# Optimization experiments

Hardware: AMD Instinct MI355X
Metric: run time of the kernel (lower is better)

## Reference

```python
import jax, jax.numpy as jnp
import numpy as np

B, Q, C, H, L, P, DFF, EXTRA = 4, 64, 384, 6, 5, 4, 1024, 128
SIZES = [(14, 14), (28, 28), (56, 56), (112, 112), (224, 224)]
S = sum(h * w for h, w in SIZES)
DH = C // H


def setup_inputs() -> dict:
    key = jax.random.key(0)
    ks = iter(jax.random.split(key, 64))
    rn = lambda shape, s=1.0: jax.random.normal(next(ks), shape, jnp.float32) * s
    inp = dict(
        tgt=rn((B, Q, C)),
        reference_points=jax.random.uniform(next(ks), (B, Q, 2), dtype=jnp.float32),
        src=rn((B, S, C)),
        extra_memory=rn((B, EXTRA, C)),
        src_valid_ratios=jnp.ones((B, L, 2), jnp.float32),
        src_spatial_shapes=jnp.asarray(SIZES, jnp.int32),
        src_level_start_index=jnp.asarray(np.cumsum([0] + [h * w for h, w in SIZES])[:-1], jnp.int32),
    )
    for name, shape in [("sa_in_w", (3 * C, C)), ("sa_out_w", (C, C)),
                        ("ea_in_w", (3 * C, C)), ("ea_out_w", (C, C)),
                        ("ms_off_w", (H * L * P * 2, C)), ("ms_attn_w", (H * L * P, C)),
                        ("ms_val_w", (C, C)), ("ms_out_w", (C, C)),
                        ("ffn_w1", (DFF, C)), ("ffn_w2", (C, DFF))]:
        inp[name] = rn(shape, 0.02)
    for name, n in [("sa_in_b", 3 * C), ("sa_out_b", C), ("ea_in_b", 3 * C), ("ea_out_b", C),
                    ("ms_attn_b", H * L * P), ("ms_val_b", C), ("ms_out_b", C),
                    ("ffn_b1", DFF), ("ffn_b2", C),
                    ("ln2_b", C), ("lne_b", C), ("ln1_b", C), ("ln3_b", C)]:
        inp[name] = jnp.zeros((n,), jnp.float32)
    inp["ms_off_b"] = rn((H * L * P * 2,), 0.5)  # nonzero so sampling is off-grid
    for name in ["ln2_g", "lne_g", "ln1_g", "ln3_g"]:
        inp[name] = jnp.ones((C,), jnp.float32)
    return inp


def layer_norm(x, g, b, eps=1e-5):
    mu = x.mean(-1, keepdims=True)
    var = ((x - mu) ** 2).mean(-1, keepdims=True)
    return (x - mu) / jnp.sqrt(var + eps) * g + b


def mha(q_in, k_in, v_in, in_w, in_b, out_w, out_b):
    d = q_in.shape[-1]
    wq, wk, wv = in_w[:d], in_w[d:2 * d], in_w[2 * d:]
    bq, bk, bv = in_b[:d], in_b[d:2 * d], in_b[2 * d:]
    proj = lambda x, w, bias: (x @ w.T + bias).reshape(x.shape[0], x.shape[1], H, DH)
    q = proj(q_in, wq, bq)
    k = proj(k_in, wk, bk)
    v = proj(v_in, wv, bv)
    scores = jnp.einsum('bqhd,bkhd->bhqk', q, k) * (1.0 / np.sqrt(DH))
    a = jax.nn.softmax(scores, axis=-1)
    o = jnp.einsum('bhqk,bkhd->bqhd', a, v).reshape(q_in.shape[0], q_in.shape[1], d)
    return o @ out_w.T + out_b


def bilinear_sample(img, x, y):
    # img [N,Hh,Ww,D]; x,y [N,M] in pixel coords; zeros padding (grid_sample align_corners=False)
    N, Hh, Ww, D = img.shape
    x0 = jnp.floor(x)
    y0 = jnp.floor(y)
    wx = (x - x0)[..., None]
    wy = (y - y0)[..., None]
    rows = jnp.arange(N)[:, None]

    def g(xi, yi):
        valid = (xi >= 0) & (xi <= Ww - 1) & (yi >= 0) & (yi <= Hh - 1)
        xc = jnp.clip(xi, 0, Ww - 1).astype(jnp.int32)
        yc = jnp.clip(yi, 0, Hh - 1).astype(jnp.int32)
        return img[rows, yc, xc] * valid[..., None]

    v00 = g(x0, y0)
    v01 = g(x0 + 1, y0)
    v10 = g(x0, y0 + 1)
    v11 = g(x0 + 1, y0 + 1)
    top = v00 * (1 - wx) + v01 * wx
    bot = v10 * (1 - wx) + v11 * wx
    return top * (1 - wy) + bot * wy


def ms_deform_attn(query, ref_pts, src, spatial, lsi,
                   off_w, off_b, aw_w, aw_b, val_w, val_b, out_w, out_b):
    # query [B,Q,C], ref_pts [B,Q,L,2] normalized
    value = (src @ val_w.T + val_b).reshape(B, S, H, DH)
    off = (query @ off_w.T + off_b).reshape(B, Q, H, L, P, 2)
    aw = jax.nn.softmax((query @ aw_w.T + aw_b).reshape(B, Q, H, L * P), -1).reshape(B, Q, H, L, P)
    normalizer = jnp.asarray([[w_, h_] for h_, w_ in spatial], jnp.float32)  # [L,2] (W,H)
    loc = ref_pts[:, :, None, :, None, :] + off / normalizer[None, None, None, :, None, :]
    out = jnp.zeros((B, Q, H, DH), jnp.float32)
    for l, (h_, w_) in enumerate(spatial):
        h_, w_ = int(h_), int(w_)
        s0 = int(lsi[l])
        v_l = value[:, s0:s0 + h_ * w_].transpose(0, 2, 1, 3).reshape(B * H, h_, w_, DH)
        xy = loc[:, :, :, l].transpose(0, 2, 1, 3, 4).reshape(B * H, Q * P, 2)
        x = xy[..., 0] * w_ - 0.5
        y = xy[..., 1] * h_ - 0.5
        samp = bilinear_sample(v_l, x, y).reshape(B, H, Q, P, DH)
        out = out + jnp.einsum('bhqpd,bqhp->bqhd', samp, aw[:, :, :, l])
    return out.reshape(B, Q, C) @ out_w.T + out_b


def reference(tgt, reference_points, src, extra_memory, src_valid_ratios,
              src_spatial_shapes, src_level_start_index,
              sa_in_w, sa_in_b, sa_out_w, sa_out_b,
              ea_in_w, ea_in_b, ea_out_w, ea_out_b,
              ms_off_w, ms_off_b, ms_attn_w, ms_attn_b,
              ms_val_w, ms_val_b, ms_out_w, ms_out_b,
              ffn_w1, ffn_b1, ffn_w2, ffn_b2,
              ln2_g, ln2_b, lne_g, lne_b, ln1_g, ln1_b, ln3_g, ln3_b):
    spatial = np.asarray(jax.device_get(src_spatial_shapes))
    lsi = np.asarray(jax.device_get(src_level_start_index))
    # reference_points_input = ref[:, :, None] * valid_ratios[:, None] -> [B,Q,L,2]
    rp_in = reference_points[:, :, None] * src_valid_ratios[:, None]
    # self attention (query_pos is None)
    t2 = mha(tgt, tgt, tgt, sa_in_w, sa_in_b, sa_out_w, sa_out_b)
    tgt = layer_norm(tgt + t2, ln2_g, ln2_b)
    # extra cross attention over concatenated first/previous memory
    t2 = mha(tgt, extra_memory, extra_memory, ea_in_w, ea_in_b, ea_out_w, ea_out_b)
    tgt = layer_norm(tgt + t2, lne_g, lne_b)
    # multi-scale deformable cross attention
    t2 = ms_deform_attn(tgt, rp_in, src, spatial, lsi,
                        ms_off_w, ms_off_b, ms_attn_w, ms_attn_b,
                        ms_val_w, ms_val_b, ms_out_w, ms_out_b)
    tgt = layer_norm(tgt + t2, ln1_g, ln1_b)
    # FFN
    t2 = jax.nn.relu(tgt @ ffn_w1.T + ffn_b1) @ ffn_w2.T + ffn_b2
    tgt = layer_norm(tgt + t2, ln3_g, ln3_b)
    return tgt
```

## Files before the change

### kernel.cpp

```cpp
#include <hip/hip_runtime.h>
#include <hip/hip_bf16.h>

#define B_ 4
#define Q_ 64
#define C_ 384
#define H_ 6
#define L_ 5
#define P_ 4
#define DFF_ 1024
#define EXTRA_ 128
#define DH_ 64
#define S_ 66836

#define FLAG_RELU 1
#define FLAG_RES 2

__device__ __forceinline__ float wave_sum(float v) {
    for (int off = 32; off; off >>= 1) v += __shfl_xor(v, off);
    return v;
}
__device__ __forceinline__ float wave_max(float v) {
    for (int off = 32; off; off >>= 1) v = fmaxf(v, __shfl_xor(v, off));
    return v;
}

__global__ __launch_bounds__(256) void lin16_kernel(
        const float* __restrict__ in, const float* __restrict__ W,
        const float* __restrict__ bias, const float* __restrict__ res,
        float* __restrict__ out, int K, int OUT, int flags) {
    extern __shared__ float xs[];
    int t = threadIdx.x;
    int r0 = blockIdx.y * 16;
    int K4 = K >> 2;
    const float4* in4 = reinterpret_cast<const float4*>(in + (size_t)r0 * K);
    float4* xs4 = reinterpret_cast<float4*>(xs);
    for (int i = t; i < 16 * K4; i += 256) xs4[i] = in4[i];
    __syncthreads();
    int j = blockIdx.x * 64 + (t & 63);
    int rg = t >> 6;
    if (j >= OUT) return;
    const float4* wp = reinterpret_cast<const float4*>(W + (size_t)j * K);
    const float4* x0 = reinterpret_cast<const float4*>(xs + (rg * 4 + 0) * K);
    const float4* x1 = reinterpret_cast<const float4*>(xs + (rg * 4 + 1) * K);
    const float4* x2 = reinterpret_cast<const float4*>(xs + (rg * 4 + 2) * K);
    const float4* x3 = reinterpret_cast<const float4*>(xs + (rg * 4 + 3) * K);
    float a0 = 0.f, a1 = 0.f, a2 = 0.f, a3 = 0.f;
#pragma unroll 4
    for (int k = 0; k < K4; ++k) {
        float4 w = wp[k];
        float4 v0 = x0[k], v1 = x1[k], v2 = x2[k], v3 = x3[k];
        a0 += w.x * v0.x + w.y * v0.y + w.z * v0.z + w.w * v0.w;
        a1 += w.x * v1.x + w.y * v1.y + w.z * v1.z + w.w * v1.w;
        a2 += w.x * v2.x + w.y * v2.y + w.z * v2.z + w.w * v2.w;
        a3 += w.x * v3.x + w.y * v3.y + w.z * v3.z + w.w * v3.w;
    }
    float bb = bias[j];
    float v[4] = {a0 + bb, a1 + bb, a2 + bb, a3 + bb};
    int orow = r0 + rg * 4;
#pragma unroll
    for (int i = 0; i < 4; ++i) {
        float o = v[i];
        if (flags & FLAG_RES) o += res[(size_t)(orow + i) * OUT + j];
        if (flags & FLAG_RELU) o = fmaxf(o, 0.f);
        out[(size_t)(orow + i) * OUT + j] = o;
    }
}

__global__ __launch_bounds__(256) void prep_kernel(
        const float* __restrict__ in, const float* __restrict__ Woff,
        const float* __restrict__ boff, const float* __restrict__ Wa,
        const float* __restrict__ ba, float* __restrict__ offs,
        float* __restrict__ lg) {
    extern __shared__ float xs[];
    int t = threadIdx.x;
    int r0 = blockIdx.y * 16;
    const float4* in4 = reinterpret_cast<const float4*>(in + (size_t)r0 * 384);
    float4* xs4 = reinterpret_cast<float4*>(xs);
    for (int i = t; i < 16 * 96; i += 256) xs4[i] = in4[i];
    __syncthreads();
    int j = blockIdx.x * 64 + (t & 63);
    int rg = t >> 6;
    if (j >= 360) return;
    const float4* wp;
    float bb;
    if (j < 240) { wp = reinterpret_cast<const float4*>(Woff + (size_t)j * 384); bb = boff[j]; }
    else         { wp = reinterpret_cast<const float4*>(Wa + (size_t)(j - 240) * 384); bb = ba[j - 240]; }
    const float4* x0 = reinterpret_cast<const float4*>(xs + (rg * 4 + 0) * 384);
    const float4* x1 = reinterpret_cast<const float4*>(xs + (rg * 4 + 1) * 384);
    const float4* x2 = reinterpret_cast<const float4*>(xs + (rg * 4 + 2) * 384);
    const float4* x3 = reinterpret_cast<const float4*>(xs + (rg * 4 + 3) * 384);
    float a0 = 0.f, a1 = 0.f, a2 = 0.f, a3 = 0.f;
#pragma unroll 4
    for (int k = 0; k < 96; ++k) {
        float4 w = wp[k];
        float4 v0 = x0[k], v1 = x1[k], v2 = x2[k], v3 = x3[k];
        a0 += w.x * v0.x + w.y * v0.y + w.z * v0.z + w.w * v0.w;
        a1 += w.x * v1.x + w.y * v1.y + w.z * v1.z + w.w * v1.w;
        a2 += w.x * v2.x + w.y * v2.y + w.z * v2.z + w.w * v2.w;
        a3 += w.x * v3.x + w.y * v3.y + w.z * v3.z + w.w * v3.w;
    }
    float v[4] = {a0 + bb, a1 + bb, a2 + bb, a3 + bb};
    int orow = r0 + rg * 4;
#pragma unroll
    for (int i = 0; i < 4; ++i) {
        if (j < 240) offs[(size_t)(orow + i) * 240 + j] = v[i];
        else         lg[(size_t)(orow + i) * 120 + (j - 240)] = v[i];
    }
}

__global__ __launch_bounds__(384) void sa_attn_kernel(const float* __restrict__ qkv,
                                                      float* __restrict__ o) {
    int row = blockIdx.x;
    int b = row >> 6;
    int t = threadIdx.x;
    int h = t >> 6, lane = t & 63;
    __shared__ float q_lds[384], a_lds[384];
    q_lds[t] = qkv[(size_t)row * 1152 + t];
    __syncthreads();
    const float* krow = qkv + (size_t)(b * 64 + lane) * 1152 + 384 + h * 64;
    float s = 0.f;
#pragma unroll 8
    for (int d = 0; d < 64; ++d) s += q_lds[h * 64 + d] * krow[d];
    s *= 0.125f;
    float m = wave_max(s);
    float e = __expf(s - m);
    float sum = wave_sum(e);
    a_lds[t] = e / sum;
    __syncthreads();
    float acc = 0.f;
#pragma unroll 4
    for (int k = 0; k < 64; ++k)
        acc += a_lds[h * 64 + k] * qkv[(size_t)(b * 64 + k) * 1152 + 768 + h * 64 + lane];
    o[(size_t)row * 384 + t] = acc;
}

__global__ __launch_bounds__(384) void ea_attn_kernel(const float* __restrict__ q,
                                                      const float* __restrict__ kv,
                                                      float* __restrict__ o) {
    int row = blockIdx.x;
    int b = row >> 6;
    int t = threadIdx.x;
    int h = t >> 6, lane = t & 63;
    __shared__ float q_lds[384], a_lds[768];
    q_lds[t] = q[(size_t)row * 384 + t];
    __syncthreads();
    const float* k0 = kv + (size_t)(b * 128 + lane) * 768 + h * 64;
    const float* k1 = k0 + (size_t)64 * 768;
    float s0 = 0.f, s1 = 0.f;
#pragma unroll 8
    for (int d = 0; d < 64; ++d) { float qd = q_lds[h * 64 + d]; s0 += qd * k0[d]; s1 += qd * k1[d]; }
    s0 *= 0.125f; s1 *= 0.125f;
    float m = wave_max(fmaxf(s0, s1));
    float e0 = __expf(s0 - m), e1 = __expf(s1 - m);
    float sum = wave_sum(e0 + e1);
    a_lds[h * 128 + lane] = e0 / sum;
    a_lds[h * 128 + 64 + lane] = e1 / sum;
    __syncthreads();
    float acc = 0.f;
#pragma unroll 4
    for (int k = 0; k < 128; ++k)
        acc += a_lds[h * 128 + k] * kv[(size_t)(b * 128 + k) * 768 + 384 + h * 64 + lane];
    o[(size_t)row * 384 + t] = acc;
}

__global__ __launch_bounds__(64) void ln_kernel(const float* __restrict__ z,
                                                const float* __restrict__ g,
                                                const float* __restrict__ beta,
                                                float* __restrict__ out) {
    int row = blockIdx.x;
    int t = threadIdx.x;
    float v[6];
    float mean = 0.f;
#pragma unroll
    for (int i = 0; i < 6; ++i) {
        v[i] = z[(size_t)row * C_ + t + i * 64];
        mean += v[i];
    }
    mean = wave_sum(mean) * (1.f / C_);
    float var = 0.f;
#pragma unroll
    for (int i = 0; i < 6; ++i) { float d = v[i] - mean; var += d * d; }
    var = wave_sum(var) * (1.f / C_);
    float inv = rsqrtf(var + 1e-5f);
#pragma unroll
    for (int i = 0; i < 6; ++i) {
        int c = t + i * 64;
        out[(size_t)row * C_ + c] = (v[i] - mean) * inv * g[c] + beta[c];
    }
}

__global__ __launch_bounds__(128) void ms_gather_kernel(
        const float* __restrict__ src, const float* __restrict__ refp,
        const float* __restrict__ vr, const float* __restrict__ offs,
        const float* __restrict__ lg, float* __restrict__ pagg,
        float* __restrict__ pwsum) {
    int l = blockIdx.x, h = blockIdx.y, row = blockIdx.z;
    int b = row >> 6;
    int t = threadIdx.x;
    const int lsi[5] = {0, 196, 980, 4116, 16660};
    const int whl[5] = {14, 28, 56, 112, 224};
    int wh = whl[l];
    float Wf = (float)wh;
    const float* lp = lg + (size_t)row * 120 + h * 20;
    float m = -1e30f;
#pragma unroll
    for (int k = 0; k < 20; ++k) m = fmaxf(m, lp[k]);
    float denom = 0.f;
#pragma unroll
    for (int k = 0; k < 20; ++k) denom += __expf(lp[k] - m);
    float dinv = 1.f / denom;
    float rpx = refp[row * 2 + 0] * vr[(b * 5 + l) * 2 + 0];
    float rpy = refp[row * 2 + 1] * vr[(b * 5 + l) * 2 + 1];
    const float* srcb = src + ((size_t)b * S_ + lsi[l]) * 384;
    float acc0 = 0.f, acc1 = 0.f, acc2 = 0.f, wsm = 0.f;
#pragma unroll
    for (int p = 0; p < 4; ++p) {
        int oidx = row * 240 + ((h * 5 + l) * 4 + p) * 2;
        float ox = offs[oidx], oy = offs[oidx + 1];
        float x = (rpx + ox / Wf) * Wf - 0.5f;
        float y = (rpy + oy / Wf) * Wf - 0.5f;
        float x0 = floorf(x), y0 = floorf(y);
        float wx = x - x0, wy = y - y0;
        float a = __expf(lp[l * 4 + p] - m) * dinv;
        float cw[4] = {(1.f - wx) * (1.f - wy), wx * (1.f - wy), (1.f - wx) * wy, wx * wy};
        float cx[4] = {x0, x0 + 1.f, x0, x0 + 1.f};
        float cy[4] = {y0, y0, y0 + 1.f, y0 + 1.f};
#pragma unroll
        for (int c2 = 0; c2 < 4; ++c2) {
            bool valid = (cx[c2] >= 0.f) && (cx[c2] <= Wf - 1.f) &&
                         (cy[c2] >= 0.f) && (cy[c2] <= Wf - 1.f);
            if (!valid) continue;
            float w = a * cw[c2];
            wsm += w;
            int xi = (int)cx[c2], yi = (int)cy[c2];
            const float* sp = srcb + (size_t)(yi * wh + xi) * 384;
            acc0 += w * sp[t];
            acc1 += w * sp[t + 128];
            acc2 += w * sp[t + 256];
        }
    }
    float* ap = pagg + ((size_t)(row * 6 + h) * 5 + l) * 384;
    ap[t] = acc0; ap[t + 128] = acc1; ap[t + 256] = acc2;
    if (t == 0) pwsum[(row * 6 + h) * 5 + l] = wsm;
}

__global__ __launch_bounds__(256) void valproj_kernel(
        const float* __restrict__ pagg, const float* __restrict__ pwsum,
        const float* __restrict__ Wv, const float* __restrict__ bv,
        float* __restrict__ val) {
    __shared__ float xs[16 * 384];
    __shared__ float ws16[16];
    int t = threadIdx.x;
    int h = blockIdx.x;
    int r0 = blockIdx.y * 16;
    float4* xs4 = reinterpret_cast<float4*>(xs);
    for (int i = t; i < 16 * 96; i += 256) {
        int row = i / 96, c4 = i % 96;
        const float4* pp = reinterpret_cast<const float4*>(pagg) +
                           ((size_t)((r0 + row) * 6 + h) * 5) * 96 + c4;
        float4 s = pp[0];
        float4 p1 = pp[96], p2 = pp[192], p3 = pp[288], p4 = pp[384];
        s.x += p1.x + p2.x + p3.x + p4.x;
        s.y += p1.y + p2.y + p3.y + p4.y;
        s.z += p1.z + p2.z + p3.z + p4.z;
        s.w += p1.w + p2.w + p3.w + p4.w;
        xs4[i] = s;
    }
    if (t < 16) {
        const float* pw = pwsum + ((size_t)(r0 + t) * 6 + h) * 5;
        ws16[t] = pw[0] + pw[1] + pw[2] + pw[3] + pw[4];
    }
    __syncthreads();
    int j = h * 64 + (t & 63);
    int rg = t >> 6;
    const float4* wp = reinterpret_cast<const float4*>(Wv + (size_t)j * 384);
    const float4* x0 = reinterpret_cast<const float4*>(xs + (rg * 4 + 0) * 384);
    const float4* x1 = reinterpret_cast<const float4*>(xs + (rg * 4 + 1) * 384);
    const float4* x2 = reinterpret_cast<const float4*>(xs + (rg * 4 + 2) * 384);
    const float4* x3 = reinterpret_cast<const float4*>(xs + (rg * 4 + 3) * 384);
    float a0 = 0.f, a1 = 0.f, a2 = 0.f, a3 = 0.f;
#pragma unroll 4
    for (int k = 0; k < 96; ++k) {
        float4 w = wp[k];
        float4 v0 = x0[k], v1 = x1[k], v2 = x2[k], v3 = x3[k];
        a0 += w.x * v0.x + w.y * v0.y + w.z * v0.z + w.w * v0.w;
        a1 += w.x * v1.x + w.y * v1.y + w.z * v1.z + w.w * v1.w;
        a2 += w.x * v2.x + w.y * v2.y + w.z * v2.z + w.w * v2.w;
        a3 += w.x * v3.x + w.y * v3.y + w.z * v3.z + w.w * v3.w;
    }
    float bb = bv[j];
    int orow = r0 + rg * 4;
    float acc[4] = {a0, a1, a2, a3};
#pragma unroll
    for (int i = 0; i < 4; ++i)
        val[(size_t)(orow + i) * 384 + j] = acc[i] + bb * ws16[rg * 4 + i];
}

extern "C" void kernel_launch(void* const* d_in, const int* in_sizes, int n_in,
                              void* d_out, int out_size, void* d_ws, size_t ws_size,
                              hipStream_t stream) {
    const float* tgt   = (const float*)d_in[0];
    const float* refp  = (const float*)d_in[1];
    const float* src   = (const float*)d_in[2];
    const float* extra = (const float*)d_in[3];
    const float* vr    = (const float*)d_in[4];
    const float* sa_in_w  = (const float*)d_in[7];
    const float* sa_out_w = (const float*)d_in[8];
    const float* ea_in_w  = (const float*)d_in[9];
    const float* ea_out_w = (const float*)d_in[10];
    const float* ms_off_w = (const float*)d_in[11];
    const float* ms_attn_w= (const float*)d_in[12];
    const float* ms_val_w = (const float*)d_in[13];
    const float* ms_out_w = (const float*)d_in[14];
    const float* ffn_w1   = (const float*)d_in[15];
    const float* ffn_w2   = (const float*)d_in[16];
    const float* sa_in_b  = (const float*)d_in[17];
    const float* sa_out_b = (const float*)d_in[18];
    const float* ea_in_b  = (const float*)d_in[19];
    const float* ea_out_b = (const float*)d_in[20];
    const float* ms_attn_b= (const float*)d_in[21];
    const float* ms_val_b = (const float*)d_in[22];
    const float* ms_out_b = (const float*)d_in[23];
    const float* ffn_b1   = (const float*)d_in[24];
    const float* ffn_b2   = (const float*)d_in[25];
    const float* ln2_b    = (const float*)d_in[26];
    const float* lne_b    = (const float*)d_in[27];
    const float* ln1_b    = (const float*)d_in[28];
    const float* ln3_b    = (const float*)d_in[29];
    const float* ms_off_b = (const float*)d_in[30];
    const float* ln2_g    = (const float*)d_in[31];
    const float* lne_g    = (const float*)d_in[32];
    const float* ln1_g    = (const float*)d_in[33];
    const float* ln3_g    = (const float*)d_in[34];

    float* ws = (float*)d_ws;
    float* s_qkv  = ws;
    float* s_eakv = ws + 294912;
    float* s_osa  = ws + 688128;
    float* s_z    = ws + 786432;
    float* s_t1   = ws + 884736;
    float* s_eaq  = ws + 983040;
    float* s_oea  = ws + 1081344;
    float* s_t2   = ws + 1179648;
    float* s_off  = ws + 1277952;
    float* s_lg   = ws + 1339392;
    float* s_pagg = ws + 1370112;
    float* s_pws  = ws + 4319232;
    float* s_val  = ws + 4326912;
    float* s_t3   = ws + 4425216;
    float* s_h1   = ws + 4523520;

    const size_t LDS384 = 16 * 384 * 4;
    const size_t LDS1024 = 16 * 1024 * 4;

    lin16_kernel<<<dim3(18, 16), 256, LDS384, stream>>>(tgt, sa_in_w, sa_in_b, nullptr, s_qkv, 384, 1152, 0);
    lin16_kernel<<<dim3(12, 32), 256, LDS384, stream>>>(extra, ea_in_w + (size_t)C_ * C_, ea_in_b + C_, nullptr, s_eakv, 384, 768, 0);
    sa_attn_kernel<<<dim3(256), dim3(384), 0, stream>>>(s_qkv, s_osa);
    lin16_kernel<<<dim3(6, 16), 256, LDS384, stream>>>(s_osa, sa_out_w, sa_out_b, tgt, s_z, 384, 384, FLAG_RES);
    ln_kernel<<<dim3(256), dim3(64), 0, stream>>>(s_z, ln2_g, ln2_b, s_t1);
    lin16_kernel<<<dim3(6, 16), 256, LDS384, stream>>>(s_t1, ea_in_w, ea_in_b, nullptr, s_eaq, 384, 384, 0);
    ea_attn_kernel<<<dim3(256), dim3(384), 0, stream>>>(s_eaq, s_eakv, s_oea);
    lin16_kernel<<<dim3(6, 16), 256, LDS384, stream>>>(s_oea, ea_out_w, ea_out_b, s_t1, s_z, 384, 384, FLAG_RES);
    ln_kernel<<<dim3(256), dim3(64), 0, stream>>>(s_z, lne_g, lne_b, s_t2);
    prep_kernel<<<dim3(6, 16), 256, LDS384, stream>>>(s_t2, ms_off_w, ms_off_b, ms_attn_w, ms_attn_b, s_off, s_lg);
    ms_gather_kernel<<<dim3(5, 6, 256), dim3(128), 0, stream>>>(src, refp, vr, s_off, s_lg, s_pagg, s_pws);
    valproj_kernel<<<dim3(6, 16), 256, 0, stream>>>(s_pagg, s_pws, ms_val_w, ms_val_b, s_val);
    lin16_kernel<<<dim3(6, 16), 256, LDS384, stream>>>(s_val, ms_out_w, ms_out_b, s_t2, s_z, 384, 384, FLAG_RES);
    ln_kernel<<<dim3(256), dim3(64), 0, stream>>>(s_z, ln1_g, ln1_b, s_t3);
    lin16_kernel<<<dim3(16, 16), 256, LDS384, stream>>>(s_t3, ffn_w1, ffn_b1, nullptr, s_h1, 384, 1024, FLAG_RELU);
    lin16_kernel<<<dim3(6, 16), 256, LDS1024, stream>>>(s_h1, ffn_w2, ffn_b2, s_t3, s_z, 1024, 384, FLAG_RES);
    ln_kernel<<<dim3(256), dim3(64), 0, stream>>>(s_z, ln3_g, ln3_b, (float*)d_out);
}
```

Before: 296.5 us.

## Fuse attention blocks with output projection, residual and layernorm into per-row kernels

Merges the self-attention and extra-memory input projections into one launch, and fuses each attention stage (query projection, attention, output projection, residual add, layernorm) into a single per-row kernel. It also merges the value projection, output projection and layernorm of the deformable attention into one per-row kernel. The goal is fewer launches and fewer round trips of intermediates through global memory. In exchange, each row block rereads the full 384x384 weight matrices, 256 blocks in total, with no reuse across rows, so weight traffic rises and the GEMV-style matmuls become less efficient.

Result: faster. 268.2 us (-9.5%).

```diff
diff --git a/kernel.cpp b/kernel.cpp
--- a/kernel.cpp
+++ b/kernel.cpp
@@ -23,30 +23,42 @@
     for (int off = 32; off; off >>= 1) v = fmaxf(v, __shfl_xor(v, off));
     return v;
 }
-
-__global__ __launch_bounds__(256) void lin16_kernel(
-        const float* __restrict__ in, const float* __restrict__ W,
-        const float* __restrict__ bias, const float* __restrict__ res,
-        float* __restrict__ out, int K, int OUT, int flags) {
-    extern __shared__ float xs[];
-    int t = threadIdx.x;
-    int r0 = blockIdx.y * 16;
-    int K4 = K >> 2;
-    const float4* in4 = reinterpret_cast<const float4*>(in + (size_t)r0 * K);
+__device__ __forceinline__ float block_sum6(float v, float* red, int t) {
+    v = wave_sum(v);
+    if ((t & 63) == 0) red[t >> 6] = v;
+    __syncthreads();
+    float s = red[0] + red[1] + red[2] + red[3] + red[4] + red[5];
+    __syncthreads();
+    return s;
+}
+
+__global__ __launch_bounds__(256) void proj_kernel(
+        const float* __restrict__ tgt, const float* __restrict__ extra,
+        const float* __restrict__ Wqkv, const float* __restrict__ bqkv,
+        const float* __restrict__ Wkv, const float* __restrict__ bkv,
+        float* __restrict__ qkv, float* __restrict__ eakv) {
+    __shared__ float xs[16 * 384];
+    int t = threadIdx.x;
+    int bx = blockIdx.x;
+    const float *in, *W, *bias;
+    float* out;
+    int OUT, r0, xt;
+    if (bx < 288) { xt = bx % 18; r0 = (bx / 18) * 16; in = tgt;   W = Wqkv; bias = bqkv; out = qkv;  OUT = 1152; }
+    else { int b2 = bx - 288; xt = b2 % 12; r0 = (b2 / 12) * 16; in = extra; W = Wkv;  bias = bkv;  out = eakv; OUT = 768; }
+    const float4* in4 = reinterpret_cast<const float4*>(in + (size_t)r0 * 384);
     float4* xs4 = reinterpret_cast<float4*>(xs);
-    for (int i = t; i < 16 * K4; i += 256) xs4[i] = in4[i];
-    __syncthreads();
-    int j = blockIdx.x * 64 + (t & 63);
+    for (int i = t; i < 16 * 96; i += 256) xs4[i] = in4[i];
+    __syncthreads();
+    int j = xt * 64 + (t & 63);
     int rg = t >> 6;
-    if (j >= OUT) return;
-    const float4* wp = reinterpret_cast<const float4*>(W + (size_t)j * K);
-    const float4* x0 = reinterpret_cast<const float4*>(xs + (rg * 4 + 0) * K);
-    const float4* x1 = reinterpret_cast<const float4*>(xs + (rg * 4 + 1) * K);
-    const float4* x2 = reinterpret_cast<const float4*>(xs + (rg * 4 + 2) * K);
-    const float4* x3 = reinterpret_cast<const float4*>(xs + (rg * 4 + 3) * K);
+    const float4* wp = reinterpret_cast<const float4*>(W + (size_t)j * 384);
+    const float4* x0 = reinterpret_cast<const float4*>(xs + (rg * 4 + 0) * 384);
+    const float4* x1 = reinterpret_cast<const float4*>(xs + (rg * 4 + 1) * 384);
+    const float4* x2 = reinterpret_cast<const float4*>(xs + (rg * 4 + 2) * 384);
+    const float4* x3 = reinterpret_cast<const float4*>(xs + (rg * 4 + 3) * 384);
     float a0 = 0.f, a1 = 0.f, a2 = 0.f, a3 = 0.f;
 #pragma unroll 4
-    for (int k = 0; k < K4; ++k) {
+    for (int k = 0; k < 96; ++k) {
         float4 w = wp[k];
         float4 v0 = x0[k], v1 = x1[k], v2 = x2[k], v3 = x3[k];
         a0 += w.x * v0.x + w.y * v0.y + w.z * v0.z + w.w * v0.w;
@@ -58,12 +70,101 @@
     float v[4] = {a0 + bb, a1 + bb, a2 + bb, a3 + bb};
     int orow = r0 + rg * 4;
 #pragma unroll
-    for (int i = 0; i < 4; ++i) {
-        float o = v[i];
-        if (flags & FLAG_RES) o += res[(size_t)(orow + i) * OUT + j];
-        if (flags & FLAG_RELU) o = fmaxf(o, 0.f);
-        out[(size_t)(orow + i) * OUT + j] = o;
-    }
+    for (int i = 0; i < 4; ++i) out[(size_t)(orow + i) * OUT + j] = v[i];
+}
+
+__global__ __launch_bounds__(384) void sa_fused_kernel(
+        const float* __restrict__ qkv, const float* __restrict__ res,
+        const float* __restrict__ Wo, const float* __restrict__ bo,
+        const float* __restrict__ g, const float* __restrict__ beta,
+        float* __restrict__ out) {
+    int row = blockIdx.x;
+    int b = row >> 6;
+    int t = threadIdx.x;
+    int h = t >> 6, lane = t & 63;
+    __shared__ float q_lds[384], a_lds[384], o_lds[384], red[8];
+    q_lds[t] = qkv[(size_t)row * 1152 + t];
+    __syncthreads();
+    const float* krow = qkv + (size_t)(b * 64 + lane) * 1152 + 384 + h * 64;
+    float s = 0.f;
+#pragma unroll 8
+    for (int d = 0; d < 64; ++d) s += q_lds[h * 64 + d] * krow[d];
+    s *= 0.125f;
+    float m = wave_max(s);
+    float e = __expf(s - m);
+    float sum = wave_sum(e);
+    a_lds[t] = e / sum;
+    __syncthreads();
+    float acc = 0.f;
+#pragma unroll 4
+    for (int k = 0; k < 64; ++k)
+        acc += a_lds[h * 64 + k] * qkv[(size_t)(b * 64 + k) * 1152 + 768 + h * 64 + lane];
+    o_lds[t] = acc;
+    __syncthreads();
+    const float* wp = Wo + (size_t)t * 384;
+    float v = bo[t] + res[(size_t)row * 384 + t];
+#pragma unroll 4
+    for (int k = 0; k < 384; k += 4) {
+        float4 w = *reinterpret_cast<const float4*>(wp + k);
+        v += w.x * o_lds[k] + w.y * o_lds[k + 1] + w.z * o_lds[k + 2] + w.w * o_lds[k + 3];
+    }
+    float mean = block_sum6(v, red, t) * (1.f / 384.f);
+    float d = v - mean;
+    float var = block_sum6(d * d, red, t) * (1.f / 384.f);
+    out[(size_t)row * 384 + t] = d * rsqrtf(var + 1e-5f) * g[t] + beta[t];
+}
+
+__global__ __launch_bounds__(384) void ea_fused_kernel(
+        const float* __restrict__ t1, const float* __restrict__ kv,
+        const float* __restrict__ Wq, const float* __restrict__ bq,
+        const float* __restrict__ Wo, const float* __restrict__ bo,
+        const float* __restrict__ g, const float* __restrict__ beta,
+        float* __restrict__ out) {
+    int row = blockIdx.x;
+    int b = row >> 6;
+    int t = threadIdx.x;
+    int h = t >> 6, lane = t & 63;
+    __shared__ float in_lds[384], q_lds[384], a_lds[768], o_lds[384], red[8];
+    in_lds[t] = t1[(size_t)row * 384 + t];
+    __syncthreads();
+    const float* wq = Wq + (size_t)t * 384;
+    float qv = bq[t];
+#pragma unroll 4
+    for (int k = 0; k < 384; k += 4) {
+        float4 w = *reinterpret_cast<const float4*>(wq + k);
+        qv += w.x * in_lds[k] + w.y * in_lds[k + 1] + w.z * in_lds[k + 2] + w.w * in_lds[k + 3];
+    }
+    q_lds[t] = qv;
+    __syncthreads();
+    const float* k0 = kv + (size_t)(b * 128 + lane) * 768 + h * 64;
+    const float* k1 = k0 + (size_t)64 * 768;
+    float s0 = 0.f, s1 = 0.f;
+#pragma unroll 8
+    for (int d = 0; d < 64; ++d) { float qd = q_lds[h * 64 + d]; s0 += qd * k0[d]; s1 += qd * k1[d]; }
+    s0 *= 0.125f; s1 *= 0.125f;
+    float m = wave_max(fmaxf(s0, s1));
+    float e0 = __expf(s0 - m), e1 = __expf(s1 - m);
+    float sum = wave_sum(e0 + e1);
+    a_lds[h * 128 + lane] = e0 / sum;
+    a_lds[h * 128 + 64 + lane] = e1 / sum;
+    __syncthreads();
+    float acc = 0.f;
+#pragma unroll 4
+    for (int k = 0; k < 128; ++k)
+        acc += a_lds[h * 128 + k] * kv[(size_t)(b * 128 + k) * 768 + 384 + h * 64 + lane];
+    o_lds[t] = acc;
+    __syncthreads();
+    const float* wo = Wo + (size_t)t * 384;
+    float v = bo[t] + in_lds[t];
+#pragma unroll 4
+    for (int k = 0; k < 384; k += 4) {
+        float4 w = *reinterpret_cast<const float4*>(wo + k);
+        v += w.x * o_lds[k] + w.y * o_lds[k + 1] + w.z * o_lds[k + 2] + w.w * o_lds[k + 3];
+    }
+    float mean = block_sum6(v, red, t) * (1.f / 384.f);
+    float d = v - mean;
+    float var = block_sum6(d * d, red, t) * (1.f / 384.f);
+    out[(size_t)row * 384 + t] = d * rsqrtf(var + 1e-5f) * g[t] + beta[t];
 }
 
 __global__ __launch_bounds__(256) void prep_kernel(
@@ -71,7 +172,7 @@
         const float* __restrict__ boff, const float* __restrict__ Wa,
         const float* __restrict__ ba, float* __restrict__ offs,
         float* __restrict__ lg) {
-    extern __shared__ float xs[];
+    __shared__ float xs[16 * 384];
     int t = threadIdx.x;
     int r0 = blockIdx.y * 16;
     const float4* in4 = reinterpret_cast<const float4*>(in + (size_t)r0 * 384);
@@ -108,87 +209,6 @@
     }
 }
 
-__global__ __launch_bounds__(384) void sa_attn_kernel(const float* __restrict__ qkv,
-                                                      float* __restrict__ o) {
-    int row = blockIdx.x;
-    int b = row >> 6;
-    int t = threadIdx.x;
-    int h = t >> 6, lane = t & 63;
-    __shared__ float q_lds[384], a_lds[384];
-    q_lds[t] = qkv[(size_t)row * 1152 + t];
-    __syncthreads();
-    const float* krow = qkv + (size_t)(b * 64 + lane) * 1152 + 384 + h * 64;
-    float s = 0.f;
-#pragma unroll 8
-    for (int d = 0; d < 64; ++d) s += q_lds[h * 64 + d] * krow[d];
-    s *= 0.125f;
-    float m = wave_max(s);
-    float e = __expf(s - m);
-    float sum = wave_sum(e);
-    a_lds[t] = e / sum;
-    __syncthreads();
-    float acc = 0.f;
-#pragma unroll 4
-    for (int k = 0; k < 64; ++k)
-        acc += a_lds[h * 64 + k] * qkv[(size_t)(b * 64 + k) * 1152 + 768 + h * 64 + lane];
-    o[(size_t)row * 384 + t] = acc;
-}
-
-__global__ __launch_bounds__(384) void ea_attn_kernel(const float* __restrict__ q,
-                                                      const float* __restrict__ kv,
-                                                      float* __restrict__ o) {
-    int row = blockIdx.x;
-    int b = row >> 6;
-    int t = threadIdx.x;
-    int h = t >> 6, lane = t & 63;
-    __shared__ float q_lds[384], a_lds[768];
-    q_lds[t] = q[(size_t)row * 384 + t];
-    __syncthreads();
-    const float* k0 = kv + (size_t)(b * 128 + lane) * 768 + h * 64;
-    const float* k1 = k0 + (size_t)64 * 768;
-    float s0 = 0.f, s1 = 0.f;
-#pragma unroll 8
-    for (int d = 0; d < 64; ++d) { float qd = q_lds[h * 64 + d]; s0 += qd * k0[d]; s1 += qd * k1[d]; }
-    s0 *= 0.125f; s1 *= 0.125f;
-    float m = wave_max(fmaxf(s0, s1));
-    float e0 = __expf(s0 - m), e1 = __expf(s1 - m);
-    float sum = wave_sum(e0 + e1);
-    a_lds[h * 128 + lane] = e0 / sum;
-    a_lds[h * 128 + 64 + lane] = e1 / sum;
-    __syncthreads();
-    float acc = 0.f;
-#pragma unroll 4
-    for (int k = 0; k < 128; ++k)
-        acc += a_lds[h * 128 + k] * kv[(size_t)(b * 128 + k) * 768 + 384 + h * 64 + lane];
-    o[(size_t)row * 384 + t] = acc;
-}
-
-__global__ __launch_bounds__(64) void ln_kernel(const float* __restrict__ z,
-                                                const float* __restrict__ g,
-                                                const float* __restrict__ beta,
-                                                float* __restrict__ out) {
-    int row = blockIdx.x;
-    int t = threadIdx.x;
-    float v[6];
-    float mean = 0.f;
-#pragma unroll
-    for (int i = 0; i < 6; ++i) {
-        v[i] = z[(size_t)row * C_ + t + i * 64];
-        mean += v[i];
-    }
-    mean = wave_sum(mean) * (1.f / C_);
-    float var = 0.f;
-#pragma unroll
-    for (int i = 0; i < 6; ++i) { float d = v[i] - mean; var += d * d; }
-    var = wave_sum(var) * (1.f / C_);
-    float inv = rsqrtf(var + 1e-5f);
-#pragma unroll
-    for (int i = 0; i < 6; ++i) {
-        int c = t + i * 64;
-        out[(size_t)row * C_ + c] = (v[i] - mean) * inv * g[c] + beta[c];
-    }
-}
-
 __global__ __launch_bounds__(128) void ms_gather_kernel(
         const float* __restrict__ src, const float* __restrict__ refp,
         const float* __restrict__ vr, const float* __restrict__ offs,
@@ -244,43 +264,74 @@
     if (t == 0) pwsum[(row * 6 + h) * 5 + l] = wsm;
 }
 
-__global__ __launch_bounds__(256) void valproj_kernel(
+__global__ __launch_bounds__(384) void ms_valout_kernel(
         const float* __restrict__ pagg, const float* __restrict__ pwsum,
         const float* __restrict__ Wv, const float* __restrict__ bv,
-        float* __restrict__ val) {
-    __shared__ float xs[16 * 384];
-    __shared__ float ws16[16];
-    int t = threadIdx.x;
-    int h = blockIdx.x;
+        const float* __restrict__ Wo, const float* __restrict__ bo,
+        const float* __restrict__ t2, const float* __restrict__ g,
+        const float* __restrict__ beta, float* __restrict__ out) {
+    int row = blockIdx.x;
+    int t = threadIdx.x;
+    __shared__ float agg[2304], val[384], wsum[6], red[8];
+#pragma unroll
+    for (int e = 0; e < 6; ++e) {
+        int idx = t + e * 384;
+        int hh = idx / 384, col = idx % 384;
+        const float* pp = pagg + ((size_t)(row * 6 + hh) * 5) * 384 + col;
+        agg[idx] = pp[0] + pp[384] + pp[768] + pp[1152] + pp[1536];
+    }
+    if (t < 6) {
+        const float* pw = pwsum + (row * 6 + t) * 5;
+        wsum[t] = pw[0] + pw[1] + pw[2] + pw[3] + pw[4];
+    }
+    __syncthreads();
+    int h = t >> 6;
+    const float* wp = Wv + (size_t)t * 384;
+    const float* ag = agg + h * 384;
+    float v = bv[t] * wsum[h];
+#pragma unroll 4
+    for (int k = 0; k < 384; k += 4) {
+        float4 w = *reinterpret_cast<const float4*>(wp + k);
+        v += w.x * ag[k] + w.y * ag[k + 1] + w.z * ag[k + 2] + w.w * ag[k + 3];
+    }
+    val[t] = v;
+    __syncthreads();
+    const float* wo = Wo + (size_t)t * 384;
+    float o = bo[t] + t2[(size_t)row * 384 + t];
+#pragma unroll 4
+    for (int k = 0; k < 384; k += 4) {
+        float4 w = *reinterpret_cast<const float4*>(wo + k);
+        o += w.x * val[k] + w.y * val[k + 1] + w.z * val[k + 2] + w.w * val[k + 3];
+    }
+    float mean = block_sum6(o, red, t) * (1.f / 384.f);
+    float d = o - mean;
+    float var = block_sum6(d * d, red, t) * (1.f / 384.f);
+    out[(size_t)row * 384 + t] = d * rsqrtf(var + 1e-5f) * g[t] + beta[t];
+}
+
+__global__ __launch_bounds__(256) void lin16_kernel(
+        const float* __restrict__ in, const float* __restrict__ W,
+        const float* __restrict__ bias, const float* __restrict__ res,
+        float* __restrict__ out, int K, int OUT, int flags) {
+    extern __shared__ float xs[];
+    int t = threadIdx.x;
     int r0 = blockIdx.y * 16;
+    int K4 = K >> 2;
+    const float4* in4 = reinterpret_cast<const float4*>(in + (size_t)r0 * K);
     float4* xs4 = reinterpret_cast<float4*>(xs);
-    for (int i = t; i < 16 * 96; i += 256) {
-        int row = i / 96, c4 = i % 96;
-        const float4* pp = reinterpret_cast<const float4*>(pagg) +
-                           ((size_t)((r0 + row) * 6 + h) * 5) * 96 + c4;
-        float4 s = pp[0];
-        float4 p1 = pp[96], p2 = pp[192], p3 = pp[288], p4 = pp[384];
-        s.x += p1.x + p2.x + p3.x + p4.x;
-        s.y += p1.y + p2.y + p3.y + p4.y;
-        s.z += p1.z + p2.z + p3.z + p4.z;
-        s.w += p1.w + p2.w + p3.w + p4.w;
-        xs4[i] = s;
-    }
-    if (t < 16) {
-        const float* pw = pwsum + ((size_t)(r0 + t) * 6 + h) * 5;
-        ws16[t] = pw[0] + pw[1] + pw[2] + pw[3] + pw[4];
-    }
-    __syncthreads();
-    int j = h * 64 + (t & 63);
+    for (int i = t; i < 16 * K4; i += 256) xs4[i] = in4[i];
+    __syncthreads();
+    int j = blockIdx.x * 64 + (t & 63);
     int rg = t >> 6;
-    const float4* wp = reinterpret_cast<const float4*>(Wv + (size_t)j * 384);
-    const float4* x0 = reinterpret_cast<const float4*>(xs + (rg * 4 + 0) * 384);
-    const float4* x1 = reinterpret_cast<const float4*>(xs + (rg * 4 + 1) * 384);
-    const float4* x2 = reinterpret_cast<const float4*>(xs + (rg * 4 + 2) * 384);
-    const float4* x3 = reinterpret_cast<const float4*>(xs + (rg * 4 + 3) * 384);
+    if (j >= OUT) return;
+    const float4* wp = reinterpret_cast<const float4*>(W + (size_t)j * K);
+    const float4* x0 = reinterpret_cast<const float4*>(xs + (rg * 4 + 0) * K);
+    const float4* x1 = reinterpret_cast<const float4*>(xs + (rg * 4 + 1) * K);
+    const float4* x2 = reinterpret_cast<const float4*>(xs + (rg * 4 + 2) * K);
+    const float4* x3 = reinterpret_cast<const float4*>(xs + (rg * 4 + 3) * K);
     float a0 = 0.f, a1 = 0.f, a2 = 0.f, a3 = 0.f;
 #pragma unroll 4
-    for (int k = 0; k < 96; ++k) {
+    for (int k = 0; k < K4; ++k) {
         float4 w = wp[k];
         float4 v0 = x0[k], v1 = x1[k], v2 = x2[k], v3 = x3[k];
         a0 += w.x * v0.x + w.y * v0.y + w.z * v0.z + w.w * v0.w;
@@ -288,12 +339,42 @@
         a2 += w.x * v2.x + w.y * v2.y + w.z * v2.z + w.w * v2.w;
         a3 += w.x * v3.x + w.y * v3.y + w.z * v3.z + w.w * v3.w;
     }
-    float bb = bv[j];
+    float bb = bias[j];
+    float v[4] = {a0 + bb, a1 + bb, a2 + bb, a3 + bb};
     int orow = r0 + rg * 4;
-    float acc[4] = {a0, a1, a2, a3};
-#pragma unroll
-    for (int i = 0; i < 4; ++i)
-        val[(size_t)(orow + i) * 384 + j] = acc[i] + bb * ws16[rg * 4 + i];
+#pragma unroll
+    for (int i = 0; i < 4; ++i) {
+        float o = v[i];
+        if (flags & FLAG_RES) o += res[(size_t)(orow + i) * OUT + j];
+        if (flags & FLAG_RELU) o = fmaxf(o, 0.f);
+        out[(size_t)(orow + i) * OUT + j] = o;
+    }
+}
+
+__global__ __launch_bounds__(64) void ln_kernel(const float* __restrict__ z,
+                                                const float* __restrict__ g,
+                                                const float* __restrict__ beta,
+                                                float* __restrict__ out) {
+    int row = blockIdx.x;
+    int t = threadIdx.x;
+    float v[6];
+    float mean = 0.f;
+#pragma unroll
+    for (int i = 0; i < 6; ++i) {
+        v[i] = z[(size_t)row * C_ + t + i * 64];
+        mean += v[i];
+    }
+    mean = wave_sum(mean) * (1.f / C_);
+    float var = 0.f;
+#pragma unroll
+    for (int i = 0; i < 6; ++i) { float d = v[i] - mean; var += d * d; }
+    var = wave_sum(var) * (1.f / C_);
+    float inv = rsqrtf(var + 1e-5f);
+#pragma unroll
+    for (int i = 0; i < 6; ++i) {
+        int c = t + i * 64;
+        out[(size_t)row * C_ + c] = (v[i] - mean) * inv * g[c] + beta[c];
+    }
 }
 
 extern "C" void kernel_launch(void* const* d_in, const int* in_sizes, int n_in,
@@ -336,38 +417,27 @@
     float* ws = (float*)d_ws;
     float* s_qkv  = ws;
     float* s_eakv = ws + 294912;
-    float* s_osa  = ws + 688128;
-    float* s_z    = ws + 786432;
-    float* s_t1   = ws + 884736;
-    float* s_eaq  = ws + 983040;
-    float* s_oea  = ws + 1081344;
-    float* s_t2   = ws + 1179648;
-    float* s_off  = ws + 1277952;
-    float* s_lg   = ws + 1339392;
-    float* s_pagg = ws + 1370112;
-    float* s_pws  = ws + 4319232;
-    float* s_val  = ws + 4326912;
-    float* s_t3   = ws + 4425216;
-    float* s_h1   = ws + 4523520;
+    float* s_t1   = ws + 688128;
+    float* s_t2   = ws + 786432;
+    float* s_off  = ws + 884736;
+    float* s_lg   = ws + 946176;
+    float* s_pagg = ws + 976896;
+    float* s_pws  = ws + 3926016;
+    float* s_t3   = ws + 3933696;
+    float* s_h1   = ws + 4032000;
+    float* s_z    = ws + 4294144;
 
     const size_t LDS384 = 16 * 384 * 4;
     const size_t LDS1024 = 16 * 1024 * 4;
 
-    lin16_kernel<<<dim3(18, 16), 256, LDS384, stream>>>(tgt, sa_in_w, sa_in_b, nullptr, s_qkv, 384, 1152, 0);
-    lin16_kernel<<<dim3(12, 32), 256, LDS384, stream>>>(extra, ea_in_w + (size_t)C_ * C_, ea_in_b + C_, nullptr, s_eakv, 384, 768, 0);
-    sa_attn_kernel<<<dim3(256), dim3(384), 0, stream>>>(s_qkv, s_osa);
-    lin16_kernel<<<dim3(6, 16), 256, LDS384, stream>>>(s_osa, sa_out_w, sa_out_b, tgt, s_z, 384, 384, FLAG_RES);
-    ln_kernel<<<dim3(256), dim3(64), 0, stream>>>(s_z, ln2_g, ln2_b, s_t1);
-    lin16_kernel<<<dim3(6, 16), 256, LDS384, stream>>>(s_t1, ea_in_w, ea_in_b, nullptr, s_eaq, 384, 384, 0);
-    ea_attn_kernel<<<dim3(256), dim3(384), 0, stream>>>(s_eaq, s_eakv, s_oea);
-    lin16_kernel<<<dim3(6, 16), 256, LDS384, stream>>>(s_oea, ea_out_w, ea_out_b, s_t1, s_z, 384, 384, FLAG_RES);
-    ln_kernel<<<dim3(256), dim3(64), 0, stream>>>(s_z, lne_g, lne_b, s_t2);
-    prep_kernel<<<dim3(6, 16), 256, LDS384, stream>>>(s_t2, ms_off_w, ms_off_b, ms_attn_w, ms_attn_b, s_off, s_lg);
+    proj_kernel<<<dim3(672), dim3(256), 0, stream>>>(tgt, extra, sa_in_w, sa_in_b,
+        ea_in_w + (size_t)C_ * C_, ea_in_b + C_, s_qkv, s_eakv);
+    sa_fused_kernel<<<dim3(256), dim3(384), 0, stream>>>(s_qkv, tgt, sa_out_w, sa_out_b, ln2_g, ln2_b, s_t1);
+    ea_fused_kernel<<<dim3(256), dim3(384), 0, stream>>>(s_t1, s_eakv, ea_in_w, ea_in_b, ea_out_w, ea_out_b, lne_g, lne_b, s_t2);
+    prep_kernel<<<dim3(6, 16), dim3(256), 0, stream>>>(s_t2, ms_off_w, ms_off_b, ms_attn_w, ms_attn_b, s_off, s_lg);
     ms_gather_kernel<<<dim3(5, 6, 256), dim3(128), 0, stream>>>(src, refp, vr, s_off, s_lg, s_pagg, s_pws);
-    valproj_kernel<<<dim3(6, 16), 256, 0, stream>>>(s_pagg, s_pws, ms_val_w, ms_val_b, s_val);
-    lin16_kernel<<<dim3(6, 16), 256, LDS384, stream>>>(s_val, ms_out_w, ms_out_b, s_t2, s_z, 384, 384, FLAG_RES);
-    ln_kernel<<<dim3(256), dim3(64), 0, stream>>>(s_z, ln1_g, ln1_b, s_t3);
-    lin16_kernel<<<dim3(16, 16), 256, LDS384, stream>>>(s_t3, ffn_w1, ffn_b1, nullptr, s_h1, 384, 1024, FLAG_RELU);
-    lin16_kernel<<<dim3(6, 16), 256, LDS1024, stream>>>(s_h1, ffn_w2, ffn_b2, s_t3, s_z, 1024, 384, FLAG_RES);
+    ms_valout_kernel<<<dim3(256), dim3(384), 0, stream>>>(s_pagg, s_pws, ms_val_w, ms_val_b, ms_out_w, ms_out_b, s_t2, ln1_g, ln1_b, s_t3);
+    lin16_kernel<<<dim3(16, 16), dim3(256), LDS384, stream>>>(s_t3, ffn_w1, ffn_b1, nullptr, s_h1, 384, 1024, FLAG_RELU);
+    lin16_kernel<<<dim3(6, 16), dim3(256), LDS1024, stream>>>(s_h1, ffn_w2, ffn_b2, s_t3, s_z, 1024, 384, FLAG_RES);
     ln_kernel<<<dim3(256), dim3(64), 0, stream>>>(s_z, ln3_g, ln3_b, (float*)d_out);
 }
```
